# Kernel optimization log

Measured on AMD Instinct MI355X. Metric: run time of the kernel, lower is better.

Reference implementation:

```python
import jax, jax.numpy as jnp
import numpy as np

NEIGHBOR_N = 3


def setup_inputs() -> dict:
    key = jax.random.key(0)
    ks = jax.random.split(key, 4)
    B, D = 8192, 512
    H = D // 2
    sess_emb = jax.random.normal(ks[0], (B, D), dtype=jnp.float32)
    pool_emb = jax.random.normal(ks[1], (1024, D), dtype=jnp.float32)
    # torch Linear default init ~ U(-1/sqrt(fan_in), 1/sqrt(fan_in)); scaled normals ok as baseline
    W1 = jax.random.normal(ks[2], (D, H), dtype=jnp.float32) / np.sqrt(D)
    b1 = jnp.zeros((H,), dtype=jnp.float32)
    W2 = jax.random.normal(ks[3], (H, D), dtype=jnp.float32) / np.sqrt(H)
    b2 = jnp.zeros((D,), dtype=jnp.float32)
    return {"sess_emb": sess_emb, "pool_emb": pool_emb, "W1": W1, "b1": b1, "W2": W2, "b2": b2}


def reference(sess_emb, pool_emb, W1, b1, W2, b2):
    # scoring MLP (dropout = identity in eval mode)
    h = jax.nn.relu(sess_emb @ W1 + b1)          # (B, D/2)
    sess_proj = h @ W2 + b2                       # (B, D)
    # self-similarity and top-k neighbors
    sim_matrix = sess_proj @ sess_proj.T          # (B, B)
    cos_topk, topk_indice = jax.lax.top_k(sim_matrix, NEIGHBOR_N)  # (B, K)
    sess_topk = sess_emb[topk_indice]             # (B, K, D) gather
    cos_topk = jax.nn.softmax(cos_topk, axis=-1)  # (B, K)
    neighbor_sess = jnp.einsum('bk,bkd->bd', cos_topk, sess_topk)  # (B, D)
    return (sess_topk, neighbor_sess, cos_topk)
```

## Files before the change

### kernel.cpp

```cpp
#include <hip/hip_runtime.h>
#include <hip/hip_bf16.h>
#include <math.h>

#define NB 8192
#define DD 512
#define HH 256
#define TB 128
#define BK 32
#define KT (DD / BK)
#define NSLOT 64
#define ROWKEYS (NSLOT * 3)
#define NCAND 8
#define NTRI 2080

typedef unsigned short ushortT;
typedef __attribute__((ext_vector_type(8))) short bf16x8;
typedef __attribute__((ext_vector_type(4))) float f32x4;

#define AS1(p) ((const __attribute__((address_space(1))) void*)(p))
#define AS3(p) ((__attribute__((address_space(3))) void*)(p))

__device__ __forceinline__ ushortT bf16rne(float f) {
    unsigned u = __float_as_uint(f);
    unsigned r = u + 0x7FFFu + ((u >> 16) & 1u);
    return (ushortT)(r >> 16);
}
__device__ __forceinline__ float bf16tof(ushortT h) {
    return __uint_as_float(((unsigned)h) << 16);
}

__global__ __launch_bounds__(256)
void prep_kernel(const float* __restrict__ sess, const float* __restrict__ W1,
                 const float* __restrict__ W2,
                 ushortT* __restrict__ sess_hi, ushortT* __restrict__ sess_lo,
                 ushortT* __restrict__ w1t_hi, ushortT* __restrict__ w1t_lo,
                 ushortT* __restrict__ w2t_hi, ushortT* __restrict__ w2t_lo) {
    const int b = blockIdx.x, t = threadIdx.x;
    if (b < 2048) {
        size_t i = (size_t)b * 2048 + t * 8;
        float4 f0 = *(const float4*)&sess[i];
        float4 f1 = *(const float4*)&sess[i + 4];
        float f[8] = {f0.x, f0.y, f0.z, f0.w, f1.x, f1.y, f1.z, f1.w};
        unsigned hp[4], lp[4];
#pragma unroll
        for (int j = 0; j < 4; ++j) {
            ushortT h0 = bf16rne(f[2 * j]), h1 = bf16rne(f[2 * j + 1]);
            ushortT l0 = bf16rne(f[2 * j] - bf16tof(h0));
            ushortT l1 = bf16rne(f[2 * j + 1] - bf16tof(h1));
            hp[j] = (unsigned)h0 | ((unsigned)h1 << 16);
            lp[j] = (unsigned)l0 | ((unsigned)l1 << 16);
        }
        *(uint4*)&sess_hi[i] = *(uint4*)hp;
        *(uint4*)&sess_lo[i] = *(uint4*)lp;
    } else if (b < 2112) {
        int o = (b - 2048) * 2048 + t * 8;
        int k = o >> 8, c = o & 255;
        float4 f0 = *(const float4*)&W1[(size_t)k * 256 + c];
        float4 f1 = *(const float4*)&W1[(size_t)k * 256 + c + 4];
        float f[8] = {f0.x, f0.y, f0.z, f0.w, f1.x, f1.y, f1.z, f1.w};
#pragma unroll
        for (int j = 0; j < 8; ++j) {
            ushortT h = bf16rne(f[j]);
            w1t_hi[(size_t)(c + j) * 512 + k] = h;
            w1t_lo[(size_t)(c + j) * 512 + k] = bf16rne(f[j] - bf16tof(h));
        }
    } else {
        int o = (b - 2112) * 2048 + t * 8;
        int k = o >> 9, c = o & 511;
        float4 f0 = *(const float4*)&W2[(size_t)k * 512 + c];
        float4 f1 = *(const float4*)&W2[(size_t)k * 512 + c + 4];
        float f[8] = {f0.x, f0.y, f0.z, f0.w, f1.x, f1.y, f1.z, f1.w};
#pragma unroll
        for (int j = 0; j < 8; ++j) {
            ushortT h = bf16rne(f[j]);
            w2t_hi[(size_t)(c + j) * 256 + k] = h;
            w2t_lo[(size_t)(c + j) * 256 + k] = bf16rne(f[j] - bf16tof(h));
        }
    }
}

template <int KDIM, int NOUT, int EPI>
__global__ __launch_bounds__(256)
void mlp_gemm(const ushortT* __restrict__ Ahi, const ushortT* __restrict__ Alo,
              const ushortT* __restrict__ Bhi, const ushortT* __restrict__ Blo,
              const float* __restrict__ bias,
              ushortT* __restrict__ Ohi, ushortT* __restrict__ Olo,
              float* __restrict__ Of, ushortT* __restrict__ Ob) {
    __shared__ short gsmem[2 * 20480];
    const int KTILES = KDIM / BK;
    const int t = threadIdx.x;
    const int w = t >> 6, l = t & 63;
    const int wr = w >> 1, wc = w & 1;
    const int tx = l & 15, tg = l >> 4;
    const int rb = blockIdx.x * 64;
    const int cb = blockIdx.y * 256;

    const int rin = l >> 2;
    const int tgs = (l & 3) ^ ((rin >> 1) & 3);
    const int loff = tx * BK + ((tg ^ ((tx >> 1) & 3)) << 3);

    f32x4 acc[2][8];
#pragma unroll
    for (int i = 0; i < 2; ++i)
#pragma unroll
        for (int j = 0; j < 8; ++j) acc[i][j] = (f32x4){0.f, 0.f, 0.f, 0.f};

#define GSTAGE(buf, k0v)                                                                     \
    {                                                                                        \
        _Pragma("unroll")                                                                    \
        for (int q = 0; q < 10; ++q) {                                                       \
            int c = w * 10 + q;                                                              \
            const ushortT* src; int row; int lofs;                                           \
            if (c < 4)       { src = Ahi; row = rb + c * 16 + rin;        lofs = 0     + c * 512; }        \
            else if (c < 8)  { src = Alo; row = rb + (c - 4) * 16 + rin;  lofs = 2048  + (c - 4) * 512; }  \
            else if (c < 24) { src = Bhi; row = cb + (c - 8) * 16 + rin;  lofs = 4096  + (c - 8) * 512; }  \
            else             { src = Blo; row = cb + (c - 24) * 16 + rin; lofs = 12288 + (c - 24) * 512; } \
            const ushortT* g = src + (size_t)row * KDIM + (k0v) + tgs * 8;                   \
            __builtin_amdgcn_global_load_lds(AS1(g), AS3(gsmem + (buf) * 20480 + lofs + l * 8), 16, 0, 0); \
        }                                                                                    \
    }

#define GCOMPUTE(kt)                                                                         \
    {                                                                                        \
        const short* Bu = gsmem + ((kt) & 1) * 20480;                                        \
        bf16x8 ah[2], al[2], bh[8], bl[8];                                                   \
        _Pragma("unroll")                                                                    \
        for (int mi = 0; mi < 2; ++mi) {                                                     \
            ah[mi] = *(const bf16x8*)&Bu[0 + (wr * 2 + mi) * 512 + loff];                    \
            al[mi] = *(const bf16x8*)&Bu[2048 + (wr * 2 + mi) * 512 + loff];                 \
        }                                                                                    \
        _Pragma("unroll")                                                                    \
        for (int nj = 0; nj < 8; ++nj) {                                                     \
            bh[nj] = *(const bf16x8*)&Bu[4096 + (wc * 8 + nj) * 512 + loff];                 \
            bl[nj] = *(const bf16x8*)&Bu[12288 + (wc * 8 + nj) * 512 + loff];                \
        }                                                                                    \
        asm volatile("s_waitcnt lgkmcnt(0)" ::: "memory");                                   \
        __builtin_amdgcn_sched_barrier(0);                                                   \
        __builtin_amdgcn_s_barrier();                                                        \
        __builtin_amdgcn_sched_barrier(0);                                                   \
        _Pragma("unroll")                                                                    \
        for (int mi = 0; mi < 2; ++mi)                                                       \
            _Pragma("unroll")                                                                \
            for (int nj = 0; nj < 8; ++nj) {                                                 \
                acc[mi][nj] = __builtin_amdgcn_mfma_f32_16x16x32_bf16(ah[mi], bh[nj], acc[mi][nj], 0, 0, 0); \
                acc[mi][nj] = __builtin_amdgcn_mfma_f32_16x16x32_bf16(ah[mi], bl[nj], acc[mi][nj], 0, 0, 0); \
                acc[mi][nj] = __builtin_amdgcn_mfma_f32_16x16x32_bf16(al[mi], bh[nj], acc[mi][nj], 0, 0, 0); \
            }                                                                                \
    }

    GSTAGE(0, 0);
    for (int kt = 0; kt < KTILES - 1; ++kt) {
        GSTAGE((kt + 1) & 1, (kt + 1) * BK);
        asm volatile("s_waitcnt vmcnt(10)" ::: "memory");
        __builtin_amdgcn_sched_barrier(0);
        __builtin_amdgcn_s_barrier();
        __builtin_amdgcn_sched_barrier(0);
        GCOMPUTE(kt);
    }
    asm volatile("s_waitcnt vmcnt(0)" ::: "memory");
    __builtin_amdgcn_sched_barrier(0);
    __builtin_amdgcn_s_barrier();
    __builtin_amdgcn_sched_barrier(0);
    GCOMPUTE(KTILES - 1);
#undef GSTAGE
#undef GCOMPUTE

#pragma unroll
    for (int mi = 0; mi < 2; ++mi) {
#pragma unroll
        for (int nj = 0; nj < 8; ++nj) {
            int col = cb + wc * 128 + nj * 16 + tx;
            float bv = bias[col];
#pragma unroll
            for (int rr = 0; rr < 4; ++rr) {
                int row = rb + wr * 32 + mi * 16 + tg * 4 + rr;
                float v = acc[mi][nj][rr] + bv;
                if (EPI == 0) {
                    v = fmaxf(v, 0.f);
                    ushortT h = bf16rne(v);
                    Ohi[(size_t)row * NOUT + col] = h;
                    Olo[(size_t)row * NOUT + col] = bf16rne(v - bf16tof(h));
                } else {
                    Of[(size_t)row * NOUT + col] = v;
                    Ob[(size_t)row * NOUT + col] = bf16rne(v);
                }
            }
        }
    }
}

__device__ __forceinline__ void ins3k(unsigned key, unsigned& k0, unsigned& k1, unsigned& k2) {
    bool g0 = key > k0, g1 = key > k1, g2 = key > k2;
    k2 = g1 ? k1 : (g2 ? key : k2);
    k1 = g0 ? k0 : (g1 ? key : k1);
    k0 = g0 ? key : k0;
}
__device__ __forceinline__ void merge3k(unsigned& a0, unsigned& a1, unsigned& a2,
                                        unsigned b0, unsigned b1, unsigned b2) {
    unsigned m0 = a0 > b0 ? a0 : b0;
    bool c0 = a0 > b0;
    unsigned ca1 = c0 ? a1 : b1;
    unsigned cb0 = c0 ? b0 : a0;
    unsigned ca2 = c0 ? a2 : b2;
    unsigned cb1 = c0 ? b1 : a1;
    bool c1 = ca1 > cb0;
    unsigned m1 = c1 ? ca1 : cb0;
    unsigned x = c1 ? ca2 : ca1;
    unsigned y = c1 ? cb0 : cb1;
    unsigned m2 = x > y ? x : y;
    a0 = m0; a1 = m1; a2 = m2;
}
__device__ __forceinline__ unsigned packkey(float f, unsigned idx) {
    unsigned u = __float_as_uint(f);
    unsigned tt = (unsigned)((int)u >> 31) | 0x80000000u;
    return ((u ^ tt) & 0xFFFFE000u) | (8191u - idx);
}

__global__ __launch_bounds__(256)
void sim_mfma_kernel(const short* __restrict__ projb, unsigned* __restrict__ pkeys) {
    const int L = blockIdx.x;
    int jbk = (int)((sqrtf(8.0f * L + 1.0f) - 1.0f) * 0.5f);
    while ((jbk + 1) * (jbk + 2) / 2 <= L) ++jbk;
    while (jbk * (jbk + 1) / 2 > L) --jbk;
    const int ib = L - jbk * (jbk + 1) / 2;
    const bool do_tr = (ib < jbk);

    __shared__ short smem[2 * TB * BK * 2];
    short* As = smem;
    short* Bs = smem + 2 * TB * BK;
    unsigned* evu = (unsigned*)smem;
    unsigned* evt = (unsigned*)smem + 3200;

    const int t = threadIdx.x;
    const int w = t >> 6, l = t & 63;
    const int wr = w >> 1, wc = w & 1;
    const int tx = l & 15, tg = l >> 4;
    const int rb = ib * TB;
    const int jb = jbk * TB;

    const int rin = l >> 2;
    const int tgs = (l & 3) ^ ((rin >> 1) & 3);
    const int loff = tx * BK + ((tg ^ ((tx >> 1) & 3)) << 3);

    f32x4 acc[4][4];
#pragma unroll
    for (int i = 0; i < 4; ++i)
#pragma unroll
        for (int j = 0; j < 4; ++j) acc[i][j] = (f32x4){0.f, 0.f, 0.f, 0.f};

#define STAGE(buf, k0)                                                                      \
    {                                                                                       \
        _Pragma("unroll")                                                                   \
        for (int q = 0; q < 2; ++q) {                                                       \
            int c = w * 2 + q;                                                              \
            const short* ga = projb + (size_t)(rb + c * 16 + rin) * DD + (k0) + tgs * 8;    \
            __builtin_amdgcn_global_load_lds(AS1(ga), AS3(As + (buf) * (TB * BK) + c * 512 + l * 8), 16, 0, 0); \
            const short* gb = projb + (size_t)(jb + c * 16 + rin) * DD + (k0) + tgs * 8;    \
            __builtin_amdgcn_global_load_lds(AS1(gb), AS3(Bs + (buf) * (TB * BK) + c * 512 + l * 8), 16, 0, 0); \
        }                                                                                   \
    }

#define COMPUTE(kt)                                                                          \
    {                                                                                        \
        const short* Ab = As + ((kt) & 1) * (TB * BK);                                       \
        const short* Bb = Bs + ((kt) & 1) * (TB * BK);                                       \
        bf16x8 af[4], bfr[4];                                                                \
        _Pragma("unroll")                                                                    \
        for (int mi = 0; mi < 4; ++mi)                                                       \
            af[mi] = *(const bf16x8*)&Ab[(wr * 64 + mi * 16) * BK + loff];                   \
        _Pragma("unroll")                                                                    \
        for (int nj = 0; nj < 4; ++nj)                                                       \
            bfr[nj] = *(const bf16x8*)&Bb[(wc * 64 + nj * 16) * BK + loff];                  \
        asm volatile("s_waitcnt lgkmcnt(0)" ::: "memory");                                   \
        __builtin_amdgcn_sched_barrier(0);                                                   \
        __builtin_amdgcn_s_barrier();                                                        \
        __builtin_amdgcn_sched_barrier(0);                                                   \
        _Pragma("unroll")                                                                    \
        for (int mi = 0; mi < 4; ++mi)                                                       \
            _Pragma("unroll")                                                                \
            for (int nj = 0; nj < 4; ++nj)                                                   \
                acc[mi][nj] = __builtin_amdgcn_mfma_f32_16x16x32_bf16(af[mi], bfr[nj], acc[mi][nj], 0, 0, 0); \
    }

    STAGE(0, 0);
    for (int kt = 0; kt < KT - 1; ++kt) {
        STAGE((kt + 1) & 1, (kt + 1) * BK);
        asm volatile("s_waitcnt vmcnt(4)" ::: "memory");
        __builtin_amdgcn_sched_barrier(0);
        __builtin_amdgcn_s_barrier();
        __builtin_amdgcn_sched_barrier(0);
        COMPUTE(kt);
    }
    asm volatile("s_waitcnt vmcnt(0)" ::: "memory");
    __builtin_amdgcn_sched_barrier(0);
    __builtin_amdgcn_s_barrier();
    __builtin_amdgcn_sched_barrier(0);
    COMPUTE(KT - 1);
#undef STAGE
#undef COMPUTE

    __syncthreads();

    unsigned cinv[4];
#pragma unroll
    for (int nj = 0; nj < 4; ++nj)
        cinv[nj] = 8191u - (unsigned)(jb + wc * 64 + nj * 16 + tx);
#pragma unroll
    for (int mi = 0; mi < 4; ++mi) {
#pragma unroll
        for (int rr = 0; rr < 4; ++rr) {
            unsigned k0 = 0, k1 = 0, k2 = 0;
#pragma unroll
            for (int nj = 0; nj < 4; ++nj) {
                unsigned u = __float_as_uint(acc[mi][nj][rr]);
                unsigned tt = (unsigned)((int)u >> 31) | 0x80000000u;
                ins3k(((u ^ tt) & 0xFFFFE000u) | cinv[nj], k0, k1, k2);
            }
#pragma unroll
            for (int s = 1; s <= 2; s <<= 1) {
                unsigned b0 = (unsigned)__shfl_xor((int)k0, s, 64);
                unsigned b1 = (unsigned)__shfl_xor((int)k1, s, 64);
                unsigned b2 = (unsigned)__shfl_xor((int)k2, s, 64);
                merge3k(k0, k1, k2, b0, b1, b2);
            }
            if ((tx & 3) == 0) {
                int lrow = wr * 64 + mi * 16 + tg * 4 + rr;
                unsigned* e = &evu[lrow * 25 + (wc * 4 + (tx >> 2)) * 3];
                e[0] = k0; e[1] = k1; e[2] = k2;
            }
        }
    }

    if (do_tr) {
#pragma unroll
        for (int nj = 0; nj < 4; ++nj) {
            unsigned k0 = 0, k1 = 0, k2 = 0;
#pragma unroll
            for (int mi = 0; mi < 4; ++mi) {
#pragma unroll
                for (int rr = 0; rr < 4; ++rr) {
                    unsigned idx = (unsigned)(rb + wr * 64 + mi * 16 + tg * 4 + rr);
                    ins3k(packkey(acc[mi][nj][rr], idx), k0, k1, k2);
                }
            }
#pragma unroll
            for (int s = 16; s <= 32; s <<= 1) {
                unsigned b0 = (unsigned)__shfl_xor((int)k0, s, 64);
                unsigned b1 = (unsigned)__shfl_xor((int)k1, s, 64);
                unsigned b2 = (unsigned)__shfl_xor((int)k2, s, 64);
                merge3k(k0, k1, k2, b0, b1, b2);
            }
            if (tg == 0) {
                int col = wc * 64 + nj * 16 + tx;
                unsigned* e = &evt[col * 6 + wr * 3];
                e[0] = k0; e[1] = k1; e[2] = k2;
            }
        }
    }
    __syncthreads();

    if (t < TB) {
        unsigned k0 = 0, k1 = 0, k2 = 0;
        const unsigned* e = &evu[t * 25];
#pragma unroll
        for (int s = 0; s < 24; ++s) ins3k(e[s], k0, k1, k2);
        unsigned* pk = pkeys + (size_t)(rb + t) * ROWKEYS + jbk * 3;
        pk[0] = k0; pk[1] = k1; pk[2] = k2;
    }
    if (do_tr && t < TB) {
        unsigned k0 = 0, k1 = 0, k2 = 0;
        const unsigned* e = &evt[t * 6];
#pragma unroll
        for (int s = 0; s < 6; ++s) ins3k(e[s], k0, k1, k2);
        unsigned* pk = pkeys + (size_t)(jb + t) * ROWKEYS + ib * 3;
        pk[0] = k0; pk[1] = k1; pk[2] = k2;
    }
}

__global__ __launch_bounds__(256)
void rerank_out_kernel(const float* __restrict__ proj, const unsigned* __restrict__ pkeys,
                       const float* __restrict__ sess, float* __restrict__ out,
                       float* __restrict__ cos_out) {
    int r = blockIdx.x * 4 + (threadIdx.x >> 6);
    int t = threadIdx.x & 63;
    const unsigned* pk = pkeys + (size_t)r * ROWKEYS;
    unsigned a0 = pk[3 * t], a1 = pk[3 * t + 1], a2 = pk[3 * t + 2];
    {
        unsigned m01 = a0 > a1 ? a0 : a1, n01 = a0 > a1 ? a1 : a0;
        unsigned m2 = n01 > a2 ? n01 : a2, n2 = n01 > a2 ? a2 : n01;
        a0 = m01 > m2 ? m01 : m2;
        a1 = m01 > m2 ? m2 : m01;
        a2 = n2;
    }
    unsigned ck[NCAND];
#pragma unroll
    for (int i = 0; i < NCAND; ++i) {
        unsigned m = a0;
#pragma unroll
        for (int s = 1; s < 64; s <<= 1) {
            unsigned o = (unsigned)__shfl_xor((int)m, s, 64);
            m = m > o ? m : o;
        }
        ck[i] = m;
        if (a0 == m) { a0 = a1; a1 = a2; a2 = 0; }
    }
    int cj[NCAND];
#pragma unroll
    for (int i = 0; i < NCAND; ++i) cj[i] = 8191 - (int)(ck[i] & 0x1FFFu);

    const float* pr = proj + (size_t)r * DD;
    float myp[8];
#pragma unroll
    for (int k = 0; k < 8; ++k) myp[k] = pr[t * 8 + k];
    double part[NCAND];
#pragma unroll
    for (int i = 0; i < NCAND; ++i) {
        const float* pc = proj + (size_t)cj[i] * DD;
        double s = 0.0;
#pragma unroll
        for (int k = 0; k < 8; ++k) s += (double)myp[k] * (double)pc[t * 8 + k];
        part[i] = s;
    }
#pragma unroll
    for (int i = 0; i < NCAND; ++i) {
#pragma unroll
        for (int s = 1; s < 64; s <<= 1) part[i] += __shfl_xor(part[i], s, 64);
    }
    double bv0 = -1e300, bv1 = -1e300, bv2 = -1e300;
    int bj0 = 0x7fffffff, bj1 = 0x7fffffff, bj2 = 0x7fffffff;
#pragma unroll
    for (int i = 0; i < NCAND; ++i) {
        double v = part[i]; int j = cj[i];
        bool g2 = (v > bv2) || (v == bv2 && j < bj2);
        bool g1 = (v > bv1) || (v == bv1 && j < bj1);
        bool g0 = (v > bv0) || (v == bv0 && j < bj0);
        if (g2) {
            if (g1) {
                if (g0) { bv2 = bv1; bj2 = bj1; bv1 = bv0; bj1 = bj0; bv0 = v; bj0 = j; }
                else    { bv2 = bv1; bj2 = bj1; bv1 = v; bj1 = j; }
            } else      { bv2 = v; bj2 = j; }
        }
    }
    double e1 = exp(bv1 - bv0), e2 = exp(bv2 - bv0);
    double inv = 1.0 / (1.0 + e1 + e2);
    float w0 = (float)inv, w1 = (float)(e1 * inv), w2 = (float)(e2 * inv);
    if (t == 0) {
        cos_out[r * 3 + 0] = w0; cos_out[r * 3 + 1] = w1; cos_out[r * 3 + 2] = w2;
    }
    const float4* s0 = (const float4*)(sess + (size_t)bj0 * DD);
    const float4* s1 = (const float4*)(sess + (size_t)bj1 * DD);
    const float4* s2 = (const float4*)(sess + (size_t)bj2 * DD);
    float4* o = (float4*)(out + (size_t)r * 3 * DD);
    float4* nb = (float4*)(out + (size_t)NB * 3 * DD + (size_t)r * DD);
#pragma unroll
    for (int e = 0; e < 2; ++e) {
        int q = t + e * 64;
        float4 x0 = s0[q], x1 = s1[q], x2 = s2[q];
        o[q] = x0; o[128 + q] = x1; o[256 + q] = x2;
        float4 v;
        v.x = fmaf(w0, x0.x, fmaf(w1, x1.x, w2 * x2.x));
        v.y = fmaf(w0, x0.y, fmaf(w1, x1.y, w2 * x2.y));
        v.z = fmaf(w0, x0.z, fmaf(w1, x1.z, w2 * x2.z));
        v.w = fmaf(w0, x0.w, fmaf(w1, x1.w, w2 * x2.w));
        nb[q] = v;
    }
}

extern "C" void kernel_launch(void* const* d_in, const int* in_sizes, int n_in,
                              void* d_out, int out_size, void* d_ws, size_t ws_size,
                              hipStream_t stream) {
    const float* sess = (const float*)d_in[0];
    const float* W1 = (const float*)d_in[2];
    const float* b1 = (const float*)d_in[3];
    const float* W2 = (const float*)d_in[4];
    const float* b2 = (const float*)d_in[5];
    float* out = (float*)d_out;

    const size_t MBc = 1u << 20;
    char* W = (char*)d_ws;
    float*   proj    = (float*)W;
    ushortT* sess_hi = (ushortT*)W;
    ushortT* sess_lo = sess_hi + (size_t)NB * DD;
    ushortT* projb   = (ushortT*)(W + 16 * MBc);
    ushortT* h_hi    = (ushortT*)(W + 24 * MBc);
    ushortT* h_lo    = (ushortT*)(W + 28 * MBc);
    ushortT* w1t_hi  = (ushortT*)(W + 32 * MBc);
    ushortT* w1t_lo  = w1t_hi + 256 * 512;
    ushortT* w2t_hi  = w1t_lo + 256 * 512;
    ushortT* w2t_lo  = w2t_hi + 512 * 256;
    unsigned* pkeys  = (unsigned*)(W + 24 * MBc);

    float* cos_out = out + (size_t)NB * 3 * DD + (size_t)NB * DD;

    hipLaunchKernelGGL(prep_kernel, dim3(2176), dim3(256), 0, stream,
                       sess, W1, W2, sess_hi, sess_lo, w1t_hi, w1t_lo, w2t_hi, w2t_lo);
    hipLaunchKernelGGL((mlp_gemm<512, 256, 0>), dim3(NB / 64, 1), dim3(256), 0, stream,
                       sess_hi, sess_lo, w1t_hi, w1t_lo, b1, h_hi, h_lo, (float*)nullptr, (ushortT*)nullptr);
    hipLaunchKernelGGL((mlp_gemm<256, 512, 1>), dim3(NB / 64, 2), dim3(256), 0, stream,
                       h_hi, h_lo, w2t_hi, w2t_lo, b2, (ushortT*)nullptr, (ushortT*)nullptr, proj, projb);
    hipLaunchKernelGGL(sim_mfma_kernel, dim3(NTRI), dim3(256), 0, stream,
                       (const short*)projb, pkeys);
    hipLaunchKernelGGL(rerank_out_kernel, dim3(NB / 4), dim3(256), 0, stream,
                       proj, pkeys, sess, out, cos_out);
}
```

Measured before the change: 149.6 us.

## Deepen sim GEMM K-tile to 64, remap block order, template MLP row tile

The similarity GEMM now stages K in chunks of 64 with a new XOR swizzle, halving the number of barrier-separated pipeline iterations. Its triangular block index is remapped with an 8-way interleave, likely to spread neighbouring tiles across XCDs or L2 slices. The first MLP GEMM gets a templated row tile of 32, which doubles its grid for better CU occupancy but lowers per-block reuse of the weight tiles. The larger LDS footprint in the sim kernel may reduce occupancy.

After: 141.9 us. 1.05x faster.

```diff
diff --git a/kernel.cpp b/kernel.cpp
--- a/kernel.cpp
+++ b/kernel.cpp
@@ -7,7 +7,8 @@
 #define HH 256
 #define TB 128
 #define BK 32
-#define KT (DD / BK)
+#define BK2 64
+#define KT2 (DD / BK2)
 #define NSLOT 64
 #define ROWKEYS (NSLOT * 3)
 #define NCAND 8
@@ -79,67 +80,72 @@
     }
 }
 
-template <int KDIM, int NOUT, int EPI>
+template <int KDIM, int NOUT, int EPI, int TM>
 __global__ __launch_bounds__(256)
 void mlp_gemm(const ushortT* __restrict__ Ahi, const ushortT* __restrict__ Alo,
               const ushortT* __restrict__ Bhi, const ushortT* __restrict__ Blo,
               const float* __restrict__ bias,
               ushortT* __restrict__ Ohi, ushortT* __restrict__ Olo,
               float* __restrict__ Of, ushortT* __restrict__ Ob) {
-    __shared__ short gsmem[2 * 20480];
+    constexpr int AC = TM / 16;
+    constexpr int CHUNKS = 2 * AC + 32;
+    constexpr int QN = CHUNKS / 4;
+    constexpr int BUFS = CHUNKS * 512;
+    constexpr int MI = TM / 32;
+    __shared__ short gsmem[2 * BUFS];
     const int KTILES = KDIM / BK;
     const int t = threadIdx.x;
     const int w = t >> 6, l = t & 63;
     const int wr = w >> 1, wc = w & 1;
     const int tx = l & 15, tg = l >> 4;
-    const int rb = blockIdx.x * 64;
+    const int rb = blockIdx.x * TM;
     const int cb = blockIdx.y * 256;
 
     const int rin = l >> 2;
     const int tgs = (l & 3) ^ ((rin >> 1) & 3);
     const int loff = tx * BK + ((tg ^ ((tx >> 1) & 3)) << 3);
 
-    f32x4 acc[2][8];
-#pragma unroll
-    for (int i = 0; i < 2; ++i)
+    f32x4 acc[MI][8];
+#pragma unroll
+    for (int i = 0; i < MI; ++i)
 #pragma unroll
         for (int j = 0; j < 8; ++j) acc[i][j] = (f32x4){0.f, 0.f, 0.f, 0.f};
 
 #define GSTAGE(buf, k0v)                                                                     \
     {                                                                                        \
         _Pragma("unroll")                                                                    \
-        for (int q = 0; q < 10; ++q) {                                                       \
-            int c = w * 10 + q;                                                              \
+        for (int q = 0; q < QN; ++q) {                                                       \
+            int c = w * QN + q;                                                              \
             const ushortT* src; int row; int lofs;                                           \
-            if (c < 4)       { src = Ahi; row = rb + c * 16 + rin;        lofs = 0     + c * 512; }        \
-            else if (c < 8)  { src = Alo; row = rb + (c - 4) * 16 + rin;  lofs = 2048  + (c - 4) * 512; }  \
-            else if (c < 24) { src = Bhi; row = cb + (c - 8) * 16 + rin;  lofs = 4096  + (c - 8) * 512; }  \
-            else             { src = Blo; row = cb + (c - 24) * 16 + rin; lofs = 12288 + (c - 24) * 512; } \
+            if (c < AC)            { src = Ahi; row = rb + c * 16 + rin;             lofs = c * 512; }                  \
+            else if (c < 2 * AC)   { src = Alo; row = rb + (c - AC) * 16 + rin;      lofs = c * 512; }                  \
+            else if (c < 2*AC+16)  { src = Bhi; row = cb + (c - 2*AC) * 16 + rin;    lofs = c * 512; }                  \
+            else                   { src = Blo; row = cb + (c - 2*AC - 16) * 16 + rin; lofs = c * 512; }                \
             const ushortT* g = src + (size_t)row * KDIM + (k0v) + tgs * 8;                   \
-            __builtin_amdgcn_global_load_lds(AS1(g), AS3(gsmem + (buf) * 20480 + lofs + l * 8), 16, 0, 0); \
+            __builtin_amdgcn_global_load_lds(AS1(g), AS3(gsmem + (buf) * BUFS + lofs + l * 8), 16, 0, 0); \
         }                                                                                    \
     }
 
 #define GCOMPUTE(kt)                                                                         \
     {                                                                                        \
-        const short* Bu = gsmem + ((kt) & 1) * 20480;                                        \
-        bf16x8 ah[2], al[2], bh[8], bl[8];                                                   \
-        _Pragma("unroll")                                                                    \
-        for (int mi = 0; mi < 2; ++mi) {                                                     \
-            ah[mi] = *(const bf16x8*)&Bu[0 + (wr * 2 + mi) * 512 + loff];                    \
-            al[mi] = *(const bf16x8*)&Bu[2048 + (wr * 2 + mi) * 512 + loff];                 \
+        const short* Bu = gsmem + ((kt) & 1) * BUFS;                                         \
+        bf16x8 ah[MI], al[MI], bh[8], bl[8];                                                 \
+        _Pragma("unroll")                                                                    \
+        for (int mi = 0; mi < MI; ++mi) {                                                    \
+            ah[mi] = *(const bf16x8*)&Bu[(wr * MI + mi) * 512 + loff];                       \
+            al[mi] = *(const bf16x8*)&Bu[AC * 512 + (wr * MI + mi) * 512 + loff];            \
         }                                                                                    \
         _Pragma("unroll")                                                                    \
         for (int nj = 0; nj < 8; ++nj) {                                                     \
-            bh[nj] = *(const bf16x8*)&Bu[4096 + (wc * 8 + nj) * 512 + loff];                 \
-            bl[nj] = *(const bf16x8*)&Bu[12288 + (wc * 8 + nj) * 512 + loff];                \
+            bh[nj] = *(const bf16x8*)&Bu[2 * AC * 512 + (wc * 8 + nj) * 512 + loff];         \
+            bl[nj] = *(const bf16x8*)&Bu[(2 * AC + 16) * 512 + (wc * 8 + nj) * 512 + loff];  \
         }                                                                                    \
         asm volatile("s_waitcnt lgkmcnt(0)" ::: "memory");                                   \
         __builtin_amdgcn_sched_barrier(0);                                                   \
         __builtin_amdgcn_s_barrier();                                                        \
         __builtin_amdgcn_sched_barrier(0);                                                   \
         _Pragma("unroll")                                                                    \
-        for (int mi = 0; mi < 2; ++mi)                                                       \
+        for (int mi = 0; mi < MI; ++mi)                                                      \
             _Pragma("unroll")                                                                \
             for (int nj = 0; nj < 8; ++nj) {                                                 \
                 acc[mi][nj] = __builtin_amdgcn_mfma_f32_16x16x32_bf16(ah[mi], bh[nj], acc[mi][nj], 0, 0, 0); \
@@ -151,7 +157,8 @@
     GSTAGE(0, 0);
     for (int kt = 0; kt < KTILES - 1; ++kt) {
         GSTAGE((kt + 1) & 1, (kt + 1) * BK);
-        asm volatile("s_waitcnt vmcnt(10)" ::: "memory");
+        if constexpr (TM == 64) { asm volatile("s_waitcnt vmcnt(10)" ::: "memory"); }
+        else                    { asm volatile("s_waitcnt vmcnt(9)" ::: "memory"); }
         __builtin_amdgcn_sched_barrier(0);
         __builtin_amdgcn_s_barrier();
         __builtin_amdgcn_sched_barrier(0);
@@ -166,14 +173,14 @@
 #undef GCOMPUTE
 
 #pragma unroll
-    for (int mi = 0; mi < 2; ++mi) {
+    for (int mi = 0; mi < MI; ++mi) {
 #pragma unroll
         for (int nj = 0; nj < 8; ++nj) {
             int col = cb + wc * 128 + nj * 16 + tx;
             float bv = bias[col];
 #pragma unroll
             for (int rr = 0; rr < 4; ++rr) {
-                int row = rb + wr * 32 + mi * 16 + tg * 4 + rr;
+                int row = rb + wr * (TM / 2) + mi * 16 + tg * 4 + rr;
                 float v = acc[mi][nj][rr] + bv;
                 if (EPI == 0) {
                     v = fmaxf(v, 0.f);
@@ -218,16 +225,17 @@
 
 __global__ __launch_bounds__(256)
 void sim_mfma_kernel(const short* __restrict__ projb, unsigned* __restrict__ pkeys) {
-    const int L = blockIdx.x;
+    const int b = blockIdx.x;
+    const int L = (b & 7) * 260 + (b >> 3);
     int jbk = (int)((sqrtf(8.0f * L + 1.0f) - 1.0f) * 0.5f);
     while ((jbk + 1) * (jbk + 2) / 2 <= L) ++jbk;
     while (jbk * (jbk + 1) / 2 > L) --jbk;
     const int ib = L - jbk * (jbk + 1) / 2;
     const bool do_tr = (ib < jbk);
 
-    __shared__ short smem[2 * TB * BK * 2];
+    __shared__ short smem[2 * TB * BK2 * 2];
     short* As = smem;
-    short* Bs = smem + 2 * TB * BK;
+    short* Bs = smem + 2 * TB * BK2;
     unsigned* evu = (unsigned*)smem;
     unsigned* evt = (unsigned*)smem + 3200;
 
@@ -238,9 +246,9 @@
     const int rb = ib * TB;
     const int jb = jbk * TB;
 
-    const int rin = l >> 2;
-    const int tgs = (l & 3) ^ ((rin >> 1) & 3);
-    const int loff = tx * BK + ((tg ^ ((tx >> 1) & 3)) << 3);
+    const int sl8 = (((l & 7) ^ (l >> 3)) << 3);
+    const int sw0 = (((0 + tg) ^ (tx & 7)) << 3);
+    const int sw1 = (((4 + tg) ^ (tx & 7)) << 3);
 
     f32x4 acc[4][4];
 #pragma unroll
@@ -251,26 +259,32 @@
 #define STAGE(buf, k0)                                                                      \
     {                                                                                       \
         _Pragma("unroll")                                                                   \
-        for (int q = 0; q < 2; ++q) {                                                       \
-            int c = w * 2 + q;                                                              \
-            const short* ga = projb + (size_t)(rb + c * 16 + rin) * DD + (k0) + tgs * 8;    \
-            __builtin_amdgcn_global_load_lds(AS1(ga), AS3(As + (buf) * (TB * BK) + c * 512 + l * 8), 16, 0, 0); \
-            const short* gb = projb + (size_t)(jb + c * 16 + rin) * DD + (k0) + tgs * 8;    \
-            __builtin_amdgcn_global_load_lds(AS1(gb), AS3(Bs + (buf) * (TB * BK) + c * 512 + l * 8), 16, 0, 0); \
+        for (int q = 0; q < 4; ++q) {                                                       \
+            int c = w * 4 + q;                                                              \
+            const short* ga = projb + (size_t)(rb + c * 8 + (l >> 3)) * DD + (k0) + sl8;    \
+            __builtin_amdgcn_global_load_lds(AS1(ga), AS3(As + (buf) * 8192 + c * 512 + l * 8), 16, 0, 0); \
+            const short* gb = projb + (size_t)(jb + c * 8 + (l >> 3)) * DD + (k0) + sl8;    \
+            __builtin_amdgcn_global_load_lds(AS1(gb), AS3(Bs + (buf) * 8192 + c * 512 + l * 8), 16, 0, 0); \
         }                                                                                   \
     }
 
 #define COMPUTE(kt)                                                                          \
     {                                                                                        \
-        const short* Ab = As + ((kt) & 1) * (TB * BK);                                       \
-        const short* Bb = Bs + ((kt) & 1) * (TB * BK);                                       \
-        bf16x8 af[4], bfr[4];                                                                \
-        _Pragma("unroll")                                                                    \
-        for (int mi = 0; mi < 4; ++mi)                                                       \
-            af[mi] = *(const bf16x8*)&Ab[(wr * 64 + mi * 16) * BK + loff];                   \
-        _Pragma("unroll")                                                                    \
-        for (int nj = 0; nj < 4; ++nj)                                                       \
-            bfr[nj] = *(const bf16x8*)&Bb[(wc * 64 + nj * 16) * BK + loff];                  \
+        const short* Ab = As + ((kt) & 1) * 8192;                                            \
+        const short* Bb = Bs + ((kt) & 1) * 8192;                                            \
+        bf16x8 af0[4], af1[4], bf0[4], bf1[4];                                               \
+        _Pragma("unroll")                                                                    \
+        for (int mi = 0; mi < 4; ++mi) {                                                     \
+            int row = wr * 64 + mi * 16 + tx;                                                \
+            af0[mi] = *(const bf16x8*)&Ab[row * 64 + sw0];                                   \
+            af1[mi] = *(const bf16x8*)&Ab[row * 64 + sw1];                                   \
+        }                                                                                    \
+        _Pragma("unroll")                                                                    \
+        for (int nj = 0; nj < 4; ++nj) {                                                     \
+            int row = wc * 64 + nj * 16 + tx;                                                \
+            bf0[nj] = *(const bf16x8*)&Bb[row * 64 + sw0];                                   \
+            bf1[nj] = *(const bf16x8*)&Bb[row * 64 + sw1];                                   \
+        }                                                                                    \
         asm volatile("s_waitcnt lgkmcnt(0)" ::: "memory");                                   \
         __builtin_amdgcn_sched_barrier(0);                                                   \
         __builtin_amdgcn_s_barrier();                                                        \
@@ -279,13 +293,18 @@
         for (int mi = 0; mi < 4; ++mi)                                                       \
             _Pragma("unroll")                                                                \
             for (int nj = 0; nj < 4; ++nj)                                                   \
-                acc[mi][nj] = __builtin_amdgcn_mfma_f32_16x16x32_bf16(af[mi], bfr[nj], acc[mi][nj], 0, 0, 0); \
+                acc[mi][nj] = __builtin_amdgcn_mfma_f32_16x16x32_bf16(af0[mi], bf0[nj], acc[mi][nj], 0, 0, 0); \
+        _Pragma("unroll")                                                                    \
+        for (int mi = 0; mi < 4; ++mi)                                                       \
+            _Pragma("unroll")                                                                \
+            for (int nj = 0; nj < 4; ++nj)                                                   \
+                acc[mi][nj] = __builtin_amdgcn_mfma_f32_16x16x32_bf16(af1[mi], bf1[nj], acc[mi][nj], 0, 0, 0); \
     }
 
     STAGE(0, 0);
-    for (int kt = 0; kt < KT - 1; ++kt) {
-        STAGE((kt + 1) & 1, (kt + 1) * BK);
-        asm volatile("s_waitcnt vmcnt(4)" ::: "memory");
+    for (int kt = 0; kt < KT2 - 1; ++kt) {
+        STAGE((kt + 1) & 1, (kt + 1) * BK2);
+        asm volatile("s_waitcnt vmcnt(8)" ::: "memory");
         __builtin_amdgcn_sched_barrier(0);
         __builtin_amdgcn_s_barrier();
         __builtin_amdgcn_sched_barrier(0);
@@ -295,7 +314,7 @@
     __builtin_amdgcn_sched_barrier(0);
     __builtin_amdgcn_s_barrier();
     __builtin_amdgcn_sched_barrier(0);
-    COMPUTE(KT - 1);
+    COMPUTE(KT2 - 1);
 #undef STAGE
 #undef COMPUTE
 
@@ -494,9 +513,9 @@
 
     hipLaunchKernelGGL(prep_kernel, dim3(2176), dim3(256), 0, stream,
                        sess, W1, W2, sess_hi, sess_lo, w1t_hi, w1t_lo, w2t_hi, w2t_lo);
-    hipLaunchKernelGGL((mlp_gemm<512, 256, 0>), dim3(NB / 64, 1), dim3(256), 0, stream,
+    hipLaunchKernelGGL((mlp_gemm<512, 256, 0, 32>), dim3(NB / 32, 1), dim3(256), 0, stream,
                        sess_hi, sess_lo, w1t_hi, w1t_lo, b1, h_hi, h_lo, (float*)nullptr, (ushortT*)nullptr);
-    hipLaunchKernelGGL((mlp_gemm<256, 512, 1>), dim3(NB / 64, 2), dim3(256), 0, stream,
+    hipLaunchKernelGGL((mlp_gemm<256, 512, 1, 64>), dim3(NB / 64, 2), dim3(256), 0, stream,
                        h_hi, h_lo, w2t_hi, w2t_lo, b2, (ushortT*)nullptr, (ushortT*)nullptr, proj, projb);
     hipLaunchKernelGGL(sim_mfma_kernel, dim3(NTRI), dim3(256), 0, stream,
                        (const short*)projb, pkeys);
```
